# Kernel tuning notes

Measured on AMD Instinct MI355X. Metric: run time of the kernel, lower is better.

## Reference

```python
import math
import jax, jax.numpy as jnp
import numpy as np

DIM = 1024
NUM_HEADS = 16
HEAD_DIM = DIM // NUM_HEADS


def setup_inputs() -> dict:
    key = jax.random.key(0)
    ks = jax.random.split(key, 5)
    b, t, d = 2, 2048, DIM
    x = jax.random.normal(ks[0], (b, t, d), dtype=jnp.float32)
    mask = jnp.ones((b, t), dtype=jnp.float32)  # 1 = keep, 0 = pad
    s_in = 1.0 / math.sqrt(d)
    w_qkv = jax.random.normal(ks[1], (3 * d, d), dtype=jnp.float32) * s_in
    b_qkv = jnp.zeros((3 * d,), dtype=jnp.float32)
    w_out = jax.random.normal(ks[2], (d, d), dtype=jnp.float32) * s_in
    b_out = jnp.zeros((d,), dtype=jnp.float32)
    return {"x": x, "mask": mask, "w_qkv": w_qkv, "b_qkv": b_qkv,
            "w_out": w_out, "b_out": b_out}


def reference(x, mask, w_qkv, b_qkv, w_out, b_out):
    b, t, d = x.shape
    h, hd = NUM_HEADS, HEAD_DIM
    # qkv projection (torch Linear: x @ W^T + b)
    qkv = x @ w_qkv.T + b_qkv                          # [b,t,3d]
    q, k, v = jnp.split(qkv, 3, axis=-1)
    def reshape(z):
        return z.reshape(b, t, h, hd).transpose(0, 2, 1, 3)  # [b,h,t,hd]
    q, k, v = reshape(q), reshape(k), reshape(v)
    att = jnp.einsum('bhqd,bhkd->bhqk', q, k) / math.sqrt(hd)  # [b,h,t,t]
    causal = jnp.tril(jnp.ones((t, t), dtype=bool))            # [t,t]
    keep = causal[None, None, :, :] & (mask[:, None, None, :] != 0)
    att = jnp.where(keep, att, -jnp.inf)
    att = jax.nn.softmax(att, axis=-1)
    out = jnp.einsum('bhqk,bhkd->bhqd', att, v)        # [b,h,t,hd]
    out = out.transpose(0, 2, 1, 3).reshape(b, t, d)
    return out @ w_out.T + b_out
```

## Files before the change

### kernel.cpp

```cpp
#include <hip/hip_runtime.h>
#include <cmath>

#define B_ 2
#define T_ 2048
#define D_ 1024
#define H_ 16
#define HD_ 64
#define M_ (B_ * T_)
#define N3_ (3 * D_)
#define K_ 1024

typedef _Float16 halfx8 __attribute__((ext_vector_type(8)));
typedef _Float16 halfx4 __attribute__((ext_vector_type(4)));
typedef float f32x4 __attribute__((ext_vector_type(4)));
typedef float f32x16 __attribute__((ext_vector_type(16)));

#define ASYNC_COPY16(gp, lp) \
  __builtin_amdgcn_global_load_lds((__attribute__((address_space(1))) void*)(gp), \
      (__attribute__((address_space(3))) void*)(lp), 16, 0, 0)

#define QSCALE 0.1803368801111204f

__device__ const int QT_OF[72] = {
    15,15,15,15,15,15,15,15, 14,14,14,14,14,14,14,14,
    13,13,13,13,13,13,13, 12,12,12,12,12,12,12,
    11,11,11,11,11,11, 10,10,10,10,10,10,
    9,9,9,9,9, 8,8,8,8,8, 7,7,7,7, 6,6,6,6,
    5,5,5, 4,4,4, 3,3, 2,2, 1, 0};
__device__ const int C_OF[72] = {
    0,1,2,3,4,5,6,7, 0,1,2,3,4,5,6,7,
    0,1,2,3,4,5,6, 0,1,2,3,4,5,6,
    0,1,2,3,4,5, 0,1,2,3,4,5,
    0,1,2,3,4, 0,1,2,3,4, 0,1,2,3, 0,1,2,3,
    0,1,2, 0,1,2, 0,1, 0,1, 0, 0};
__device__ const int CB_OF[16] = {0,1,2,4,6,9,12,16,20,25,30,36,42,49,56,64};
__device__ const int NC_OF[16] = {1,1,2,2,3,3,4,4,5,5,6,6,7,7,8,8};
#define NSLOT 72
#define NPOSLOT 56

__global__ __launch_bounds__(256) void prep_all(
    const float* __restrict__ x, const float* __restrict__ wq,
    const float* __restrict__ wo, const float* __restrict__ mask,
    _Float16* __restrict__ xh, _Float16* __restrict__ wqh,
    _Float16* __restrict__ woh, float* __restrict__ kbias,
    int* __restrict__ tflags)
{
    int bid = blockIdx.x;
    if (bid >= 4096) {
        int i = (bid - 4096) * 256 + threadIdx.x;
        float mv = mask[i];
        kbias[i] = (mv != 0.f) ? 0.f : -INFINITY;
        unsigned long long bal = __ballot(mv != 0.f);
        if ((threadIdx.x & 63) == 0) tflags[i >> 6] = (bal == ~0ULL) ? 1 : 0;
        return;
    }
    const float* s; _Float16* d; int off;
    if (bid < 2048)      { s = x;  d = xh;  off = bid; }
    else if (bid < 3584) { s = wq; d = wqh; off = bid - 2048; }
    else                 { s = wo; d = woh; off = bid - 3584; }
    int i = (off * 256 + threadIdx.x) * 8;
    float4 a = *(const float4*)(s + i);
    float4 b = *(const float4*)(s + i + 4);
    halfx8 h;
    h[0] = (_Float16)a.x; h[1] = (_Float16)a.y; h[2] = (_Float16)a.z; h[3] = (_Float16)a.w;
    h[4] = (_Float16)b.x; h[5] = (_Float16)b.y; h[6] = (_Float16)b.z; h[7] = (_Float16)b.w;
    *(halfx8*)(d + i) = h;
}

__global__ __launch_bounds__(256) void gemm_qkv(
    const _Float16* __restrict__ A, const _Float16* __restrict__ Wt,
    const float* __restrict__ bias,
    _Float16* __restrict__ qh, _Float16* __restrict__ kh, _Float16* __restrict__ vth)
{
    __shared__ _Float16 As[128 * 32];
    __shared__ _Float16 Bs[128 * 32];
    const int tid = threadIdx.x;
    const int lane = tid & 63, w = tid >> 6;
    const int col = lane & 15, quad = lane >> 4;
    const int wr = w >> 1, wc = w & 1;
    const int m0 = blockIdx.y << 7, n0 = blockIdx.x << 7;

    const int c0 = w * 2, c1 = c0 + 1;
    const int r0 = c0 * 16 + (lane >> 2), r1 = c1 * 16 + (lane >> 2);
    const int ks = (lane & 3) << 3;

    f32x4 acc[4][4] = {};

    for (int k0 = 0; k0 < K_; k0 += 32) {
        ASYNC_COPY16(A  + (size_t)(m0 + r0) * K_ + k0 + ks, &As[c0 * 512]);
        ASYNC_COPY16(A  + (size_t)(m0 + r1) * K_ + k0 + ks, &As[c1 * 512]);
        ASYNC_COPY16(Wt + (size_t)(n0 + r0) * K_ + k0 + ks, &Bs[c0 * 512]);
        ASYNC_COPY16(Wt + (size_t)(n0 + r1) * K_ + k0 + ks, &Bs[c1 * 512]);
        __syncthreads();
        halfx8 af[4], bf[4];
#pragma unroll
        for (int i = 0; i < 4; ++i)
            af[i] = *(const halfx8*)&As[(wr * 64 + i * 16 + col) * 32 + quad * 8];
#pragma unroll
        for (int j = 0; j < 4; ++j)
            bf[j] = *(const halfx8*)&Bs[(wc * 64 + j * 16 + col) * 32 + quad * 8];
#pragma unroll
        for (int i = 0; i < 4; ++i)
#pragma unroll
            for (int j = 0; j < 4; ++j)
                acc[i][j] = __builtin_amdgcn_mfma_f32_16x16x32_f16(af[i], bf[j], acc[i][j], 0, 0, 0);
        __syncthreads();
    }

#pragma unroll
    for (int i = 0; i < 4; ++i) {
#pragma unroll
        for (int r = 0; r < 4; ++r) {
            int m = m0 + wr * 64 + i * 16 + quad * 4 + r;
            int bb = m >> 11, tt = m & (T_ - 1);
#pragma unroll
            for (int j = 0; j < 4; ++j) {
                int n = n0 + wc * 64 + j * 16 + col;
                float val = acc[i][j][r] + bias[n];
                int which = n >> 10, head = (n >> 6) & 15, dd = n & 63;
                if (which == 0) {
                    qh[((size_t)(bb * H_ + head) * T_ + tt) * HD_ + dd] = (_Float16)(val * QSCALE);
                } else if (which == 1) {
                    int hi = ((dd >> 3) ^ (tt & 7) ^ ((tt >> 3) & 7)) & 7;
                    int dds = (hi << 3) | (dd & 7);
                    kh[((size_t)(bb * H_ + head) * T_ + tt) * HD_ + dds] = (_Float16)val;
                } else {
                    int hi = (((tt >> 3) & 7) ^ (dd & 7) ^ ((dd >> 3) & 7)) & 7;
                    int tts = (tt & ~63) | (hi << 3) | (tt & 7);
                    vth[((size_t)(bb * H_ + head) * HD_ + dd) * T_ + tts] = (_Float16)val;
                }
            }
        }
    }
}

__global__ __launch_bounds__(256) void gemm_out(
    const _Float16* __restrict__ A, const _Float16* __restrict__ Wt,
    const float* __restrict__ bias, float* __restrict__ C)
{
    __shared__ _Float16 As[128 * 32];
    __shared__ _Float16 Bs[64 * 32];
    const int tid = threadIdx.x;
    const int lane = tid & 63, w = tid >> 6;
    const int col = lane & 15, quad = lane >> 4;
    const int m0 = blockIdx.y << 7, n0 = blockIdx.x << 6;

    const int c0 = w * 2, c1 = c0 + 1;
    const int rA0 = c0 * 16 + (lane >> 2), rA1 = c1 * 16 + (lane >> 2);
    const int rB = w * 16 + (lane >> 2);
    const int ks = (lane & 3) << 3;

    f32x4 acc[2][4] = {};

    for (int k0 = 0; k0 < K_; k0 += 32) {
        ASYNC_COPY16(A  + (size_t)(m0 + rA0) * K_ + k0 + ks, &As[c0 * 512]);
        ASYNC_COPY16(A  + (size_t)(m0 + rA1) * K_ + k0 + ks, &As[c1 * 512]);
        ASYNC_COPY16(Wt + (size_t)(n0 + rB) * K_ + k0 + ks, &Bs[w * 512]);
        __syncthreads();
        halfx8 af[2], bf[4];
#pragma unroll
        for (int i = 0; i < 2; ++i)
            af[i] = *(const halfx8*)&As[(w * 32 + i * 16 + col) * 32 + quad * 8];
#pragma unroll
        for (int j = 0; j < 4; ++j)
            bf[j] = *(const halfx8*)&Bs[(j * 16 + col) * 32 + quad * 8];
#pragma unroll
        for (int i = 0; i < 2; ++i)
#pragma unroll
            for (int j = 0; j < 4; ++j)
                acc[i][j] = __builtin_amdgcn_mfma_f32_16x16x32_f16(af[i], bf[j], acc[i][j], 0, 0, 0);
        __syncthreads();
    }

#pragma unroll
    for (int i = 0; i < 2; ++i) {
#pragma unroll
        for (int r = 0; r < 4; ++r) {
            int m = m0 + w * 32 + i * 16 + quad * 4 + r;
#pragma unroll
            for (int j = 0; j < 4; ++j) {
                int n = n0 + j * 16 + col;
                C[(size_t)m * D_ + n] = acc[i][j][r] + bias[n];
            }
        }
    }
}

__global__ __launch_bounds__(256) void attn_kernel(
    const _Float16* __restrict__ qh, const _Float16* __restrict__ kh,
    const _Float16* __restrict__ vth, const float* __restrict__ kbias,
    const int* __restrict__ tflags,
    float* __restrict__ pm, float* __restrict__ pl,
    _Float16* __restrict__ po, _Float16* __restrict__ oh)
{
    __shared__ _Float16 Ks[2][64 * 64];
    __shared__ _Float16 Vt[2][64 * 64];

    const int xi = blockIdx.x;
    const int qt = QT_OF[xi], c = C_OF[xi];
    const int h = blockIdx.y, b = blockIdx.z;
    const int tid = threadIdx.x;
    const int lane = tid & 63, w = tid >> 6;
    const int l31 = lane & 31, q2 = lane >> 5;

    const int kt0 = c * 4;
    const int ktend = min(2 * qt + 1, kt0 + 3);

    const int bh = b * H_ + h;
    const _Float16* qp = qh + (size_t)bh * T_ * HD_;
    const _Float16* kp = kh + (size_t)bh * T_ * HD_;
    const _Float16* vp = vth + (size_t)bh * HD_ * T_;
    const float* kb = kbias + (size_t)b * T_;
    const int* tf = tflags + b * 32;

    const int qbase = qt * 128 + w * 32;
    const int q_row = qbase + l31;

    halfx8 bq[4];
#pragma unroll
    for (int hc = 0; hc < 4; ++hc)
        bq[hc] = *(const halfx8*)(qp + (size_t)q_row * HD_ + hc * 16 + q2 * 8);

    float mrow = -INFINITY, lrow = 0.f;
    f32x16 oacc[2] = {};

    {
        const _Float16* ksrc = kp + (size_t)(kt0 * 64 + w * 16) * HD_;
        ASYNC_COPY16(ksrc + lane * 8, &Ks[0][(w * 16) * 64]);
        ASYNC_COPY16(ksrc + 8 * HD_ + lane * 8, &Ks[0][(w * 16 + 8) * 64]);
        const _Float16* vsrc = vp + (size_t)(w * 16 + (lane >> 3)) * T_
                                 + kt0 * 64 + (lane & 7) * 8;
        ASYNC_COPY16(vsrc, &Vt[0][(w * 16) * 64]);
        ASYNC_COPY16(vsrc + 8 * T_, &Vt[0][(w * 16 + 8) * 64]);
    }

    for (int kt = kt0; kt <= ktend; ++kt) {
        const int cur = (kt - kt0) & 1;
        __syncthreads();
        if (kt < ktend) {
            const int nb = cur ^ 1;
            const _Float16* ksrc = kp + (size_t)((kt + 1) * 64 + w * 16) * HD_;
            ASYNC_COPY16(ksrc + lane * 8, &Ks[nb][(w * 16) * 64]);
            ASYNC_COPY16(ksrc + 8 * HD_ + lane * 8, &Ks[nb][(w * 16 + 8) * 64]);
            const _Float16* vsrc = vp + (size_t)(w * 16 + (lane >> 3)) * T_
                                     + (kt + 1) * 64 + (lane & 7) * 8;
            ASYNC_COPY16(vsrc, &Vt[nb][(w * 16) * 64]);
            ASYNC_COPY16(vsrc + 8 * T_, &Vt[nb][(w * 16 + 8) * 64]);
        }
        if (kt * 64 > qbase + 31) continue;

        f32x16 sa[2];
#pragma unroll
        for (int kb2 = 0; kb2 < 2; ++kb2) {
            f32x16 a;
#pragma unroll
            for (int r = 0; r < 16; ++r) a[r] = 0.f;
#pragma unroll
            for (int hc = 0; hc < 4; ++hc) {
                int seg = (hc * 2 + q2) ^ (l31 & 7) ^ ((kb2 * 4 + (l31 >> 3)) & 7);
                halfx8 ka = *(const halfx8*)&Ks[cur][(kb2 * 32 + l31) * 64 + seg * 8];
                a = __builtin_amdgcn_mfma_f32_32x32x16_f16(ka, bq[hc], a, 0, 0, 0);
            }
            sa[kb2] = a;
        }

        float mx = sa[0][0];
#pragma unroll
        for (int r = 1; r < 16; ++r) mx = fmaxf(mx, sa[0][r]);
#pragma unroll
        for (int r = 0; r < 16; ++r) mx = fmaxf(mx, sa[1][r]);
        mx = fmaxf(mx, __shfl_xor(mx, 32, 64));
        float mold = mrow;
        float mnew = fmaxf(mold, mx);
        unsigned long long bump = __ballot(mnew > mold);
        mrow = mnew;

        const bool interior = (kt * 64 + 63 <= qbase);
        const int allkeep = tf[kt];
        halfx4 pf[2][4];
        float rsum = 0.f;
        if (interior && allkeep) {
#pragma unroll
            for (int kb2 = 0; kb2 < 2; ++kb2)
#pragma unroll
                for (int cc = 0; cc < 4; ++cc)
#pragma unroll
                    for (int j = 0; j < 4; ++j) {
                        float pv = exp2f(sa[kb2][cc * 4 + j] - mnew);
                        rsum += pv;
                        pf[kb2][cc][j] = (_Float16)pv;
                    }
        } else {
#pragma unroll
            for (int kb2 = 0; kb2 < 2; ++kb2)
#pragma unroll
                for (int cc = 0; cc < 4; ++cc)
#pragma unroll
                    for (int j = 0; j < 4; ++j) {
                        int key = kt * 64 + kb2 * 32 + j + 8 * cc + 4 * q2;
                        float add = allkeep ? 0.f : kb[key];
                        float pv = (key <= q_row) ? exp2f(sa[kb2][cc * 4 + j] + add - mnew) : 0.f;
                        rsum += pv;
                        pf[kb2][cc][j] = (_Float16)pv;
                    }
        }
        rsum += __shfl_xor(rsum, 32, 64);

        if (bump) {
            float alpha = exp2f(mold - mnew);
            lrow = lrow * alpha + rsum;
#pragma unroll
            for (int db = 0; db < 2; ++db)
#pragma unroll
                for (int r = 0; r < 16; ++r) oacc[db][r] *= alpha;
        } else {
            lrow += rsum;
        }

#pragma unroll
        for (int db = 0; db < 2; ++db)
#pragma unroll
            for (int kb2 = 0; kb2 < 2; ++kb2)
#pragma unroll
                for (int cc = 0; cc < 4; ++cc) {
                    int ck = kb2 * 4 + cc;
                    int seg = ck ^ (l31 & 7) ^ ((db * 4 + (l31 >> 3)) & 7);
                    halfx4 va = *(const halfx4*)&Vt[cur][(db * 32 + l31) * 64 + seg * 8 + q2 * 4];
                    oacc[db] = __builtin_amdgcn_mfma_f32_32x32x8f16(va, pf[kb2][cc], oacc[db], 0, 0, 0);
                }
    }

    const int qloc = w * 32 + l31;
    const int slot = bh * NSLOT + CB_OF[qt] + c;
    if (q2 == 0) {
        pm[(size_t)slot * 128 + qloc] = mrow;
        pl[(size_t)slot * 128 + qloc] = lrow;
    }
    _Float16* pob;
    if (c == 0)
        pob = oh + ((size_t)(b * T_ + qt * 128 + qloc)) * D_ + h * 64;
    else
        pob = po + ((size_t)(bh * NPOSLOT + (CB_OF[qt] - qt) + (c - 1)) * 128 + qloc) * 64;
#pragma unroll
    for (int db = 0; db < 2; ++db)
#pragma unroll
        for (int gg = 0; gg < 4; ++gg) {
            halfx4 ov;
#pragma unroll
            for (int j = 0; j < 4; ++j)
                ov[j] = (_Float16)(oacc[db][gg * 4 + j]);
            *(halfx4*)(pob + db * 32 + 8 * gg + 4 * q2) = ov;
        }
}

__global__ __launch_bounds__(256) void attn_combine(
    const float* __restrict__ pm, const float* __restrict__ pl,
    const _Float16* __restrict__ po, _Float16* __restrict__ oh)
{
    const int qt = blockIdx.x, h = blockIdx.y, b = blockIdx.z;
    const int nc = NC_OF[qt], cb = CB_OF[qt];
    const int bh = b * H_ + h;
    const int tid = threadIdx.x;
    const int r = tid >> 1, dh = tid & 1;

    const int slot0 = bh * NSLOT + cb;
    float mc[8], lc[8];
    float mstar = -INFINITY;
    for (int cc = 0; cc < nc; ++cc) {
        mc[cc] = pm[(size_t)(slot0 + cc) * 128 + r];
        lc[cc] = pl[(size_t)(slot0 + cc) * 128 + r];
        mstar = fmaxf(mstar, mc[cc]);
    }
    float lstar = 0.f, wc[8];
    for (int cc = 0; cc < nc; ++cc) {
        wc[cc] = exp2f(mc[cc] - mstar);
        lstar += wc[cc] * lc[cc];
    }

    _Float16* ohrow = oh + ((size_t)(b * T_ + qt * 128 + r)) * D_ + h * 64 + dh * 32;

    float acc[32];
    {
        float wv = wc[0];
#pragma unroll
        for (int g = 0; g < 4; ++g) {
            halfx8 hv = *(const halfx8*)(ohrow + g * 8);
#pragma unroll
            for (int j = 0; j < 8; ++j)
                acc[g * 8 + j] = wv * (float)hv[j];
        }
    }
    const int pbase = bh * NPOSLOT + (cb - qt);
    for (int cc = 1; cc < nc; ++cc) {
        const _Float16* src = po + ((size_t)(pbase + cc - 1) * 128 + r) * 64 + dh * 32;
        float wv = wc[cc];
#pragma unroll
        for (int g = 0; g < 4; ++g) {
            halfx8 hv = *(const halfx8*)(src + g * 8);
#pragma unroll
            for (int j = 0; j < 8; ++j)
                acc[g * 8 + j] += wv * (float)hv[j];
        }
    }
    float linv = 1.f / lstar;
#pragma unroll
    for (int g = 0; g < 4; ++g) {
        halfx8 ov;
#pragma unroll
        for (int j = 0; j < 8; ++j)
            ov[j] = (_Float16)(acc[g * 8 + j] * linv);
        *(halfx8*)(ohrow + g * 8) = ov;
    }
}

extern "C" void kernel_launch(void* const* d_in, const int* in_sizes, int n_in,
                              void* d_out, int out_size, void* d_ws, size_t ws_size,
                              hipStream_t stream)
{
    (void)in_sizes; (void)n_in; (void)out_size; (void)ws_size;
    const float* x     = (const float*)d_in[0];
    const float* mask  = (const float*)d_in[1];
    const float* w_qkv = (const float*)d_in[2];
    const float* b_qkv = (const float*)d_in[3];
    const float* w_out = (const float*)d_in[4];
    const float* b_out = (const float*)d_in[5];
    float* out = (float*)d_out;

    const size_t QKV1 = (size_t)B_ * H_ * T_ * HD_;
    _Float16* xh  = (_Float16*)d_ws;
    _Float16* wqh = xh  + (size_t)M_ * K_;
    _Float16* woh = wqh + (size_t)N3_ * K_;
    _Float16* qh  = woh + (size_t)D_ * K_;
    _Float16* kh  = qh  + QKV1;
    _Float16* vth = kh  + QKV1;
    _Float16* oh  = vth + QKV1;
    _Float16* po  = oh  + QKV1;
    float* kbias  = (float*)(po + (size_t)32 * NPOSLOT * 128 * 64);
    float* pm     = kbias + (size_t)B_ * T_;
    float* pl     = pm + (size_t)32 * NSLOT * 128;
    int* tflags   = (int*)(pl + (size_t)32 * NSLOT * 128);

    prep_all<<<4112, 256, 0, stream>>>(x, w_qkv, w_out, mask,
                                       xh, wqh, woh, kbias, tflags);
    gemm_qkv<<<dim3(N3_ / 128, M_ / 128), 256, 0, stream>>>(
        xh, wqh, b_qkv, qh, kh, vth);
    attn_kernel<<<dim3(72, H_, B_), 256, 0, stream>>>(
        qh, kh, vth, kbias, tflags, pm, pl, po, oh);
    attn_combine<<<dim3(16, H_, B_), 256, 0, stream>>>(
        pm, pl, po, oh);
    gemm_out<<<dim3(D_ / 64, M_ / 128), 256, 0, stream>>>(
        oh, woh, b_out, out);
}
```

Baseline: 210.9 us.

## Fuse attention combine into split-K attention via atomic tickets, widen GEMM K-tile

Removes the separate attn_combine launch. Each attention block bumps a per-(bh,qt) counter with an atomic, and the last arriving block merges the partial softmax results in place. Query tiles with a single chunk now normalize and write their output directly. Both GEMMs also switch from a 32-wide to a 64-wide K-tile, which halves the number of barrier pairs per K sweep at the cost of more LDS per block. The ticket scheme relies on threadfence ordering and on the counters being zeroed by an extra prep block on every call.

```diff
diff --git a/kernel.cpp b/kernel.cpp
--- a/kernel.cpp
+++ b/kernel.cpp
@@ -43,10 +43,15 @@
     const float* __restrict__ wo, const float* __restrict__ mask,
     _Float16* __restrict__ xh, _Float16* __restrict__ wqh,
     _Float16* __restrict__ woh, float* __restrict__ kbias,
-    int* __restrict__ tflags)
+    int* __restrict__ tflags, int* __restrict__ cnt)
 {
     int bid = blockIdx.x;
     if (bid >= 4096) {
+        if (bid == 4112) {
+            cnt[threadIdx.x] = 0;
+            cnt[threadIdx.x + 256] = 0;
+            return;
+        }
         int i = (bid - 4096) * 256 + threadIdx.x;
         float mv = mask[i];
         kbias[i] = (mv != 0.f) ? 0.f : -INFINITY;
@@ -72,38 +77,40 @@
     const float* __restrict__ bias,
     _Float16* __restrict__ qh, _Float16* __restrict__ kh, _Float16* __restrict__ vth)
 {
-    __shared__ _Float16 As[128 * 32];
-    __shared__ _Float16 Bs[128 * 32];
+    __shared__ _Float16 As[128 * 64];
+    __shared__ _Float16 Bs[128 * 64];
     const int tid = threadIdx.x;
     const int lane = tid & 63, w = tid >> 6;
     const int col = lane & 15, quad = lane >> 4;
     const int wr = w >> 1, wc = w & 1;
     const int m0 = blockIdx.y << 7, n0 = blockIdx.x << 7;
 
-    const int c0 = w * 2, c1 = c0 + 1;
-    const int r0 = c0 * 16 + (lane >> 2), r1 = c1 * 16 + (lane >> 2);
-    const int ks = (lane & 3) << 3;
-
     f32x4 acc[4][4] = {};
 
-    for (int k0 = 0; k0 < K_; k0 += 32) {
-        ASYNC_COPY16(A  + (size_t)(m0 + r0) * K_ + k0 + ks, &As[c0 * 512]);
-        ASYNC_COPY16(A  + (size_t)(m0 + r1) * K_ + k0 + ks, &As[c1 * 512]);
-        ASYNC_COPY16(Wt + (size_t)(n0 + r0) * K_ + k0 + ks, &Bs[c0 * 512]);
-        ASYNC_COPY16(Wt + (size_t)(n0 + r1) * K_ + k0 + ks, &Bs[c1 * 512]);
+    for (int k0 = 0; k0 < K_; k0 += 64) {
+#pragma unroll
+        for (int u = 0; u < 4; ++u) {
+            int ch = tid + u * 256;
+            int row = ch >> 3, seg = ch & 7;
+            ASYNC_COPY16(A  + (size_t)(m0 + row) * K_ + k0 + seg * 8, &As[ch * 8]);
+            ASYNC_COPY16(Wt + (size_t)(n0 + row) * K_ + k0 + seg * 8, &Bs[ch * 8]);
+        }
         __syncthreads();
-        halfx8 af[4], bf[4];
-#pragma unroll
-        for (int i = 0; i < 4; ++i)
-            af[i] = *(const halfx8*)&As[(wr * 64 + i * 16 + col) * 32 + quad * 8];
-#pragma unroll
-        for (int j = 0; j < 4; ++j)
-            bf[j] = *(const halfx8*)&Bs[(wc * 64 + j * 16 + col) * 32 + quad * 8];
-#pragma unroll
-        for (int i = 0; i < 4; ++i)
+#pragma unroll
+        for (int kk = 0; kk < 2; ++kk) {
+            halfx8 af[4], bf[4];
+#pragma unroll
+            for (int i = 0; i < 4; ++i)
+                af[i] = *(const halfx8*)&As[(wr * 64 + i * 16 + col) * 64 + kk * 32 + quad * 8];
 #pragma unroll
             for (int j = 0; j < 4; ++j)
-                acc[i][j] = __builtin_amdgcn_mfma_f32_16x16x32_f16(af[i], bf[j], acc[i][j], 0, 0, 0);
+                bf[j] = *(const halfx8*)&Bs[(wc * 64 + j * 16 + col) * 64 + kk * 32 + quad * 8];
+#pragma unroll
+            for (int i = 0; i < 4; ++i)
+#pragma unroll
+                for (int j = 0; j < 4; ++j)
+                    acc[i][j] = __builtin_amdgcn_mfma_f32_16x16x32_f16(af[i], bf[j], acc[i][j], 0, 0, 0);
+        }
         __syncthreads();
     }
 
@@ -138,37 +145,44 @@
     const _Float16* __restrict__ A, const _Float16* __restrict__ Wt,
     const float* __restrict__ bias, float* __restrict__ C)
 {
-    __shared__ _Float16 As[128 * 32];
-    __shared__ _Float16 Bs[64 * 32];
+    __shared__ _Float16 As[128 * 64];
+    __shared__ _Float16 Bs[64 * 64];
     const int tid = threadIdx.x;
     const int lane = tid & 63, w = tid >> 6;
     const int col = lane & 15, quad = lane >> 4;
     const int m0 = blockIdx.y << 7, n0 = blockIdx.x << 6;
 
-    const int c0 = w * 2, c1 = c0 + 1;
-    const int rA0 = c0 * 16 + (lane >> 2), rA1 = c1 * 16 + (lane >> 2);
-    const int rB = w * 16 + (lane >> 2);
-    const int ks = (lane & 3) << 3;
-
     f32x4 acc[2][4] = {};
 
-    for (int k0 = 0; k0 < K_; k0 += 32) {
-        ASYNC_COPY16(A  + (size_t)(m0 + rA0) * K_ + k0 + ks, &As[c0 * 512]);
-        ASYNC_COPY16(A  + (size_t)(m0 + rA1) * K_ + k0 + ks, &As[c1 * 512]);
-        ASYNC_COPY16(Wt + (size_t)(n0 + rB) * K_ + k0 + ks, &Bs[w * 512]);
+    for (int k0 = 0; k0 < K_; k0 += 64) {
+#pragma unroll
+        for (int u = 0; u < 4; ++u) {
+            int ch = tid + u * 256;
+            int row = ch >> 3, seg = ch & 7;
+            ASYNC_COPY16(A + (size_t)(m0 + row) * K_ + k0 + seg * 8, &As[ch * 8]);
+        }
+#pragma unroll
+        for (int u = 0; u < 2; ++u) {
+            int ch = tid + u * 256;
+            int row = ch >> 3, seg = ch & 7;
+            ASYNC_COPY16(Wt + (size_t)(n0 + row) * K_ + k0 + seg * 8, &Bs[ch * 8]);
+        }
         __syncthreads();
-        halfx8 af[2], bf[4];
-#pragma unroll
-        for (int i = 0; i < 2; ++i)
-            af[i] = *(const halfx8*)&As[(w * 32 + i * 16 + col) * 32 + quad * 8];
-#pragma unroll
-        for (int j = 0; j < 4; ++j)
-            bf[j] = *(const halfx8*)&Bs[(j * 16 + col) * 32 + quad * 8];
-#pragma unroll
-        for (int i = 0; i < 2; ++i)
+#pragma unroll
+        for (int kk = 0; kk < 2; ++kk) {
+            halfx8 af[2], bf[4];
+#pragma unroll
+            for (int i = 0; i < 2; ++i)
+                af[i] = *(const halfx8*)&As[(w * 32 + i * 16 + col) * 64 + kk * 32 + quad * 8];
 #pragma unroll
             for (int j = 0; j < 4; ++j)
-                acc[i][j] = __builtin_amdgcn_mfma_f32_16x16x32_f16(af[i], bf[j], acc[i][j], 0, 0, 0);
+                bf[j] = *(const halfx8*)&Bs[(j * 16 + col) * 64 + kk * 32 + quad * 8];
+#pragma unroll
+            for (int i = 0; i < 2; ++i)
+#pragma unroll
+                for (int j = 0; j < 4; ++j)
+                    acc[i][j] = __builtin_amdgcn_mfma_f32_16x16x32_f16(af[i], bf[j], acc[i][j], 0, 0, 0);
+        }
         __syncthreads();
     }
 
@@ -191,7 +205,8 @@
     const _Float16* __restrict__ vth, const float* __restrict__ kbias,
     const int* __restrict__ tflags,
     float* __restrict__ pm, float* __restrict__ pl,
-    _Float16* __restrict__ po, _Float16* __restrict__ oh)
+    _Float16* __restrict__ po, _Float16* __restrict__ oh,
+    int* __restrict__ cnt)
 {
     __shared__ _Float16 Ks[2][64 * 64];
     __shared__ _Float16 Vt[2][64 * 64];
@@ -205,6 +220,7 @@
 
     const int kt0 = c * 4;
     const int ktend = min(2 * qt + 1, kt0 + 3);
+    const int nc = NC_OF[qt];
 
     const int bh = b * H_ + h;
     const _Float16* qp = qh + (size_t)bh * T_ * HD_;
@@ -331,6 +347,23 @@
     }
 
     const int qloc = w * 32 + l31;
+
+    if (nc == 1) {
+        float linv = 1.f / lrow;
+        _Float16* pob = oh + ((size_t)(b * T_ + qt * 128 + qloc)) * D_ + h * 64;
+#pragma unroll
+        for (int db = 0; db < 2; ++db)
+#pragma unroll
+            for (int gg = 0; gg < 4; ++gg) {
+                halfx4 ov;
+#pragma unroll
+                for (int j = 0; j < 4; ++j)
+                    ov[j] = (_Float16)(oacc[db][gg * 4 + j] * linv);
+                *(halfx4*)(pob + db * 32 + 8 * gg + 4 * q2) = ov;
+            }
+        return;
+    }
+
     const int slot = bh * NSLOT + CB_OF[qt] + c;
     if (q2 == 0) {
         pm[(size_t)slot * 128 + qloc] = mrow;
@@ -351,64 +384,47 @@
                 ov[j] = (_Float16)(oacc[db][gg * 4 + j]);
             *(halfx4*)(pob + db * 32 + 8 * gg + 4 * q2) = ov;
         }
-}
-
-__global__ __launch_bounds__(256) void attn_combine(
-    const float* __restrict__ pm, const float* __restrict__ pl,
-    const _Float16* __restrict__ po, _Float16* __restrict__ oh)
-{
-    const int qt = blockIdx.x, h = blockIdx.y, b = blockIdx.z;
-    const int nc = NC_OF[qt], cb = CB_OF[qt];
-    const int bh = b * H_ + h;
-    const int tid = threadIdx.x;
+
+    __threadfence();
+    __shared__ int tick;
+    if (tid == 0) tick = atomicAdd(&cnt[bh * 16 + qt], 1);
+    __syncthreads();
+    if (tick != nc - 1) return;
+    __threadfence();
+
     const int r = tid >> 1, dh = tid & 1;
-
-    const int slot0 = bh * NSLOT + cb;
-    float mc[8], lc[8];
+    const int slot0 = bh * NSLOT + CB_OF[qt];
+    float wcv[8];
     float mstar = -INFINITY;
     for (int cc = 0; cc < nc; ++cc) {
-        mc[cc] = pm[(size_t)(slot0 + cc) * 128 + r];
-        lc[cc] = pl[(size_t)(slot0 + cc) * 128 + r];
-        mstar = fmaxf(mstar, mc[cc]);
-    }
-    float lstar = 0.f, wc[8];
+        float m = pm[(size_t)(slot0 + cc) * 128 + r];
+        wcv[cc] = m;
+        mstar = fmaxf(mstar, m);
+    }
+    float lstar = 0.f;
     for (int cc = 0; cc < nc; ++cc) {
-        wc[cc] = exp2f(mc[cc] - mstar);
-        lstar += wc[cc] * lc[cc];
-    }
-
+        float wv = exp2f(wcv[cc] - mstar);
+        wcv[cc] = wv;
+        lstar += wv * pl[(size_t)(slot0 + cc) * 128 + r];
+    }
+    float linv = 1.f / lstar;
     _Float16* ohrow = oh + ((size_t)(b * T_ + qt * 128 + r)) * D_ + h * 64 + dh * 32;
-
-    float acc[32];
-    {
-        float wv = wc[0];
-#pragma unroll
-        for (int g = 0; g < 4; ++g) {
-            halfx8 hv = *(const halfx8*)(ohrow + g * 8);
-#pragma unroll
-            for (int j = 0; j < 8; ++j)
-                acc[g * 8 + j] = wv * (float)hv[j];
-        }
-    }
-    const int pbase = bh * NPOSLOT + (cb - qt);
-    for (int cc = 1; cc < nc; ++cc) {
-        const _Float16* src = po + ((size_t)(pbase + cc - 1) * 128 + r) * 64 + dh * 32;
-        float wv = wc[cc];
-#pragma unroll
-        for (int g = 0; g < 4; ++g) {
-            halfx8 hv = *(const halfx8*)(src + g * 8);
-#pragma unroll
-            for (int j = 0; j < 8; ++j)
-                acc[g * 8 + j] += wv * (float)hv[j];
-        }
-    }
-    float linv = 1.f / lstar;
+    const int pbase = bh * NPOSLOT + (CB_OF[qt] - qt);
 #pragma unroll
     for (int g = 0; g < 4; ++g) {
+        float acc8[8];
+        halfx8 h0 = *(const halfx8*)(ohrow + g * 8);
+#pragma unroll
+        for (int j = 0; j < 8; ++j) acc8[j] = wcv[0] * (float)h0[j];
+        for (int cc = 1; cc < nc; ++cc) {
+            const _Float16* src = po + ((size_t)(pbase + cc - 1) * 128 + r) * 64 + dh * 32 + g * 8;
+            halfx8 hv = *(const halfx8*)src;
+#pragma unroll
+            for (int j = 0; j < 8; ++j) acc8[j] += wcv[cc] * (float)hv[j];
+        }
         halfx8 ov;
 #pragma unroll
-        for (int j = 0; j < 8; ++j)
-            ov[j] = (_Float16)(acc[g * 8 + j] * linv);
+        for (int j = 0; j < 8; ++j) ov[j] = (_Float16)(acc8[j] * linv);
         *(halfx8*)(ohrow + g * 8) = ov;
     }
 }
@@ -439,15 +455,14 @@
     float* pm     = kbias + (size_t)B_ * T_;
     float* pl     = pm + (size_t)32 * NSLOT * 128;
     int* tflags   = (int*)(pl + (size_t)32 * NSLOT * 128);
-
-    prep_all<<<4112, 256, 0, stream>>>(x, w_qkv, w_out, mask,
-                                       xh, wqh, woh, kbias, tflags);
+    int* cnt      = tflags + 64;
+
+    prep_all<<<4113, 256, 0, stream>>>(x, w_qkv, w_out, mask,
+                                       xh, wqh, woh, kbias, tflags, cnt);
     gemm_qkv<<<dim3(N3_ / 128, M_ / 128), 256, 0, stream>>>(
         xh, wqh, b_qkv, qh, kh, vth);
     attn_kernel<<<dim3(72, H_, B_), 256, 0, stream>>>(
-        qh, kh, vth, kbias, tflags, pm, pl, po, oh);
-    attn_combine<<<dim3(16, H_, B_), 256, 0, stream>>>(
-        pm, pl, po, oh);
+        qh, kh, vth, kbias, tflags, pm, pl, po, oh, cnt);
     gemm_out<<<dim3(D_ / 64, M_ / 128), 256, 0, stream>>>(
         oh, woh, b_out, out);
 }
```

New measurement: 831.8 us. 3.94x slower.
